# Performance work log

Measured on AMD Instinct MI355X. Metric: run time of the kernel, lower is better.

Reference implementation:

```python
import jax, jax.numpy as jnp
import numpy as np

N_ATOMS = 4096
HSIZE = 128
N_HEADS = 8
D_K = HSIZE // N_HEADS


def setup_inputs() -> dict:
    key = jax.random.key(0)
    ks = jax.random.split(key, 11)
    s = 1.0 / np.sqrt(HSIZE)
    return {
        "query": jax.random.normal(ks[0], (N_ATOMS, HSIZE), dtype=jnp.float32),
        "key": jax.random.normal(ks[1], (N_ATOMS, HSIZE), dtype=jnp.float32),
        "value": jax.random.normal(ks[2], (N_ATOMS, HSIZE), dtype=jnp.float32),
        "mask": jax.random.randint(ks[3], (N_ATOMS, N_ATOMS), 0, 2, dtype=jnp.int32),
        "Wq": jax.random.normal(ks[4], (HSIZE, HSIZE), dtype=jnp.float32) * s,
        "bq": jnp.zeros((HSIZE,), dtype=jnp.float32),
        "Wk": jax.random.normal(ks[5], (HSIZE, HSIZE), dtype=jnp.float32) * s,
        "bk": jnp.zeros((HSIZE,), dtype=jnp.float32),
        "Wv": jax.random.normal(ks[6], (HSIZE, HSIZE), dtype=jnp.float32) * s,
        "bv": jnp.zeros((HSIZE,), dtype=jnp.float32),
        "Wo": jax.random.normal(ks[7], (HSIZE, HSIZE), dtype=jnp.float32) * s,
    }


def _mha(query, key, value, mask, Wq, bq, Wk, bk, Wv, bv, Wo):
    n = query.shape[0]
    # project and split heads: [n, hsize] -> [H, n, d_k]
    def heads(x, W, b):
        return (x @ W.T + b).reshape(n, N_HEADS, D_K).transpose(1, 0, 2)
    q = heads(query, Wq, bq)
    k = heads(key, Wk, bk)
    v = heads(value, Wv, bv)
    scale = 1.0 / jnp.sqrt(jnp.asarray(D_K, q.dtype))
    scores = jnp.einsum("hnd,hmd->hnm", q, k) * scale  # [H, n, n]
    scores = jnp.where(mask[None, :, :] == 0, jnp.asarray(-1e9, scores.dtype), scores)
    p_attn = jax.nn.softmax(scores, axis=-1)
    x = jnp.einsum("hnm,hmd->hnd", p_attn, v)  # [H, n, d_k]
    x = x.transpose(1, 0, 2).reshape(n, HSIZE)  # merge heads
    return x @ Wo.T  # output_linear has bias=False


def reference(query, key, value, mask, Wq, bq, Wk, bk, Wv, bv, Wo):
    return _mha(query, key, value, mask, Wq, bq, Wk, bk, Wv, bv, Wo)
```

## Files before the change

### kernel.cpp

```cpp
#include <hip/hip_runtime.h>

#define NA 4096
#define HS 128
#define PSTR 72
#define CSTR 136

typedef unsigned short u16;
typedef unsigned long long u64;
using bf16x8  = __attribute__((ext_vector_type(8))) short;
using f32x4   = __attribute__((ext_vector_type(4))) float;
using ushort8 = __attribute__((ext_vector_type(8))) unsigned short;

#define QSCALE 0.18033688011112042f

static __device__ __forceinline__ u16 f2bf(float f) {
    unsigned u = __builtin_bit_cast(unsigned, f);
    u += 0x7FFFu + ((u >> 16) & 1u);
    return (u16)(u >> 16);
}

__global__ __launch_bounds__(256) void cvt_w(
    const float* __restrict__ Wq, const float* __restrict__ Wk,
    const float* __restrict__ Wv, const float* __restrict__ Wo,
    const float* __restrict__ bq, const float* __restrict__ bk,
    const float* __restrict__ bv,
    u16* __restrict__ Wf, float* __restrict__ bb)
{
    const int gid = blockIdx.x * 256 + threadIdx.x;
    const int e = gid * 4;
    const int mat = e >> 14, off = e & 16383;
    const float* src = (mat == 0) ? Wq : (mat == 1) ? Wk : (mat == 2) ? Wv : Wo;
    const float s = (mat == 0) ? QSCALE : 1.0f;
    float4 v = *(const float4*)(src + off);
    ushort4 o;
    o.x = f2bf(v.x * s); o.y = f2bf(v.y * s);
    o.z = f2bf(v.z * s); o.w = f2bf(v.w * s);
    const int j = off >> 7, k0 = off & 127;
    const int j0 = j >> 4, c = j & 15, kk = k0 >> 5, q = (k0 >> 3) & 3;
    const int tgt = mat * 16384 + ((j0 * 4 + kk) * 16 + c) * 32 + q * 8 + (k0 & 7);
    *(ushort4*)(Wf + tgt) = o;
    if (gid < 128)      bb[gid] = bq[gid] * QSCALE;
    else if (gid < 256) bb[gid] = bk[gid - 128];
    else if (gid < 384) bb[gid] = bv[gid - 256];
}

__global__ __launch_bounds__(256) void proj_mfma(
    const float* __restrict__ Xq, const float* __restrict__ Xk, const float* __restrict__ Xv,
    const u16* __restrict__ Wf, const float* __restrict__ bb,
    u16* __restrict__ Qbh, u16* __restrict__ Kbh, u16* __restrict__ VtB)
{
    const int mat = blockIdx.y;
    const float* X = (mat == 0) ? Xq : (mat == 1) ? Xk : Xv;
    const u16* Wm = Wf + mat * 16384;
    const float* bm = bb + mat * 128;
    const int r0b = blockIdx.x * 32;

    __shared__ __align__(16) u16 Xs[32 * CSTR];
    __shared__ __align__(16) u16 Cs[32 * CSTR];

    const int t = threadIdx.x;

    {
        const int r = t >> 3, cb = (t & 7) * 16;
        const float* Xr = X + (size_t)(r0b + r) * HS + cb;
#pragma unroll
        for (int seg = 0; seg < 4; ++seg) {
            float4 f = *(const float4*)(Xr + seg * 4);
            ushort4 u;
            u.x = f2bf(f.x); u.y = f2bf(f.y); u.z = f2bf(f.z); u.w = f2bf(f.w);
            *(ushort4*)(Xs + r * CSTR + cb + seg * 4) = u;
        }
    }
    __syncthreads();

    const int wv = t >> 6, lane = t & 63;
    const int c = lane & 15, q = lane >> 4;
    const int rw = (wv & 1) * 16;
    const int j0b = (wv >> 1) * 4;

    bf16x8 af[4];
#pragma unroll
    for (int kk = 0; kk < 4; ++kk)
        af[kk] = *(const bf16x8*)(Xs + (rw + c) * CSTR + kk * 32 + q * 8);

    const f32x4 zero = {0.f, 0.f, 0.f, 0.f};
#pragma unroll
    for (int jj = 0; jj < 4; ++jj) {
        const int j0 = j0b + jj;
        f32x4 acc = zero;
#pragma unroll
        for (int kk = 0; kk < 4; ++kk) {
            bf16x8 bf = *(const bf16x8*)(Wm + (j0 * 4 + kk) * 512 + c * 32 + q * 8);
            acc = __builtin_amdgcn_mfma_f32_16x16x32_bf16(af[kk], bf, acc, 0, 0, 0);
        }
        const float bias = bm[j0 * 16 + c];
#pragma unroll
        for (int r = 0; r < 4; ++r)
            Cs[(rw + 4 * q + r) * CSTR + j0 * 16 + c] = f2bf(acc[r] + bias);
    }
    __syncthreads();

    if (mat < 2) {
        u16* dst = (mat == 0) ? Qbh : Kbh;
        const int h8 = t >> 5, r = t & 31;
        const u16* src = Cs + r * CSTR + h8 * 16;
        u16* dp = dst + (size_t)h8 * (NA * 16) + (size_t)(r0b + r) * 16;
        *(bf16x8*)(dp)     = *(const bf16x8*)(src);
        *(bf16x8*)(dp + 8) = *(const bf16x8*)(src + 8);
    } else {
        const int d = t >> 1, s = t & 1;
        const int kb = r0b >> 6, ko = (r0b & 32) + s * 16;
        ushort8 v0, v1;
#pragma unroll
        for (int jj = 0; jj < 8; ++jj) v0[jj] = Cs[(s * 16 + jj) * CSTR + d];
#pragma unroll
        for (int jj = 0; jj < 8; ++jj) v1[jj] = Cs[(s * 16 + 8 + jj) * CSTR + d];
        u16* dp = VtB + (size_t)kb * 8192 + d * 64 + ko;
        *(ushort8*)(dp)     = v0;
        *(ushort8*)(dp + 8) = v1;
    }
}

__global__ __launch_bounds__(512, 8) void attn(
    const int* __restrict__ mask,
    const u16* __restrict__ Qbh, const u16* __restrict__ Kbh, const u16* __restrict__ VtB,
    float* __restrict__ part)
{
    __shared__ __align__(16) u16 Pbuf[8 * 16 * PSTR];
    __shared__ __align__(8)  u64 Mwp[16 * 17];

    const int t = threadIdx.x;
    const int h = t >> 6;
    const int lane = t & 63;
    const int c = lane & 15;
    const int q = lane >> 4;
    const int tile = blockIdx.x, split = blockIdx.y;
    const int i0 = tile * 16;
    const int kt0 = split * 1024;

#pragma unroll 4
    for (int rr = 0; rr < 32; ++rr) {
        const int idx = h * 32 + rr;
        const int row = idx >> 4, wc = idx & 15;
        const int v = mask[(size_t)(i0 + row) * NA + kt0 + wc * 64 + lane];
        u64 b = __ballot(v != 0);
        if (lane == 0) Mwp[row * 17 + wc] = b;
    }

    const u16* Qh = Qbh + (size_t)h * (NA * 16);
    const u16* Kh = Kbh + (size_t)h * (NA * 16);

    const bf16x8 qf = *(const bf16x8*)(Qh + (size_t)(i0 + c) * 16 + (q & 1) * 8);

    __syncthreads();

    const f32x4 zero = {0.f, 0.f, 0.f, 0.f};
    f32x4 Oacc = zero;
    float lsum = 0.f;
    u16* Pw = Pbuf + h * 16 * PSTR;

#pragma unroll 1
    for (int it = 0; it < 16; ++it) {
        const int kt = kt0 + it * 64;
        const u16* Vb = VtB + (size_t)(kt >> 6) * 8192 + (h * 16 + c) * 64;

        f32x4 ST[4];
#pragma unroll
        for (int t4 = 0; t4 < 4; ++t4) {
            bf16x8 kf = *(const bf16x8*)(Kh + (size_t)(kt + t4 * 16 + c) * 16 + (q & 1) * 8);
            ST[t4] = __builtin_amdgcn_mfma_f32_16x16x32_bf16(kf, qf, zero, 0, 0, 0);
        }
        bf16x8 vf0 = *(const bf16x8*)(Vb + q * 8);
        bf16x8 vf1 = *(const bf16x8*)(Vb + 32 + q * 8);

        u64 w = Mwp[c * 17 + it] >> (4 * q);
        unsigned mlo = (unsigned)w, mhi = (unsigned)(w >> 32);

#pragma unroll
        for (int t4 = 0; t4 < 4; ++t4) {
            const unsigned mw = (t4 < 2) ? mlo : mhi;
            const int sh = (t4 & 1) * 16;
            float p0 = ((mw >> (sh + 0)) & 1) ? __builtin_amdgcn_exp2f(ST[t4][0]) : 0.f;
            float p1 = ((mw >> (sh + 1)) & 1) ? __builtin_amdgcn_exp2f(ST[t4][1]) : 0.f;
            float p2 = ((mw >> (sh + 2)) & 1) ? __builtin_amdgcn_exp2f(ST[t4][2]) : 0.f;
            float p3 = ((mw >> (sh + 3)) & 1) ? __builtin_amdgcn_exp2f(ST[t4][3]) : 0.f;
            lsum += (p0 + p1) + (p2 + p3);
            unsigned lo = ((__builtin_bit_cast(unsigned, p0) + 0x8000u) >> 16)
                        | ((__builtin_bit_cast(unsigned, p1) + 0x8000u) & 0xFFFF0000u);
            unsigned hi = ((__builtin_bit_cast(unsigned, p2) + 0x8000u) >> 16)
                        | ((__builtin_bit_cast(unsigned, p3) + 0x8000u) & 0xFFFF0000u);
            *(uint2*)(Pw + c * PSTR + t4 * 16 + 4 * q) = make_uint2(lo, hi);
        }
        __asm__ volatile("" ::: "memory");
        __builtin_amdgcn_s_waitcnt(0xC07F);
        __asm__ volatile("" ::: "memory");

        bf16x8 pf0 = *(const bf16x8*)(Pw + c * PSTR + q * 8);
        bf16x8 pf1 = *(const bf16x8*)(Pw + c * PSTR + 32 + q * 8);
        Oacc = __builtin_amdgcn_mfma_f32_16x16x32_bf16(pf0, vf0, Oacc, 0, 0, 0);
        Oacc = __builtin_amdgcn_mfma_f32_16x16x32_bf16(pf1, vf1, Oacc, 0, 0, 0);
    }

    lsum += __shfl_xor(lsum, 16, 64);
    lsum += __shfl_xor(lsum, 32, 64);

    float* base = part + (size_t)((tile * 4 + split) * 8 + h) * 272;
#pragma unroll
    for (int r = 0; r < 4; ++r)
        base[(4 * q + r) * 16 + c] = Oacc[r];
    if (q == 0) base[256 + c] = lsum;
}

__global__ __launch_bounds__(256) void reduce_out(
    const float* __restrict__ part, const u16* __restrict__ Wf,
    float* __restrict__ out)
{
    __shared__ __align__(16) u16 xs[16 * CSTR];

    const int t = threadIdx.x;
    const int tile = blockIdx.x;
    const int i0 = tile * 16;
    const float* Pt = part + (size_t)tile * 4 * 8 * 272;

    {
        const int i = t >> 4, d = t & 15;
#pragma unroll
        for (int h = 0; h < 8; ++h) {
            float os = 0.f, ls = 0.f;
#pragma unroll
            for (int s = 0; s < 4; ++s) {
                const float* b = Pt + (size_t)(s * 8 + h) * 272;
                os += b[i * 16 + d];
                ls += b[256 + i];
            }
            xs[i * CSTR + h * 16 + d] = f2bf(os / ls);
        }
    }
    __syncthreads();

    const int wv = t >> 6, lane = t & 63;
    const int c = lane & 15, q = lane >> 4;
    const u16* WoB = Wf + 3 * 16384;

    bf16x8 af[4];
#pragma unroll
    for (int kk = 0; kk < 4; ++kk)
        af[kk] = *(const bf16x8*)(xs + c * CSTR + kk * 32 + q * 8);

    const f32x4 zero = {0.f, 0.f, 0.f, 0.f};
#pragma unroll
    for (int jj = 0; jj < 2; ++jj) {
        const int j0 = wv * 2 + jj;
        f32x4 acc = zero;
#pragma unroll
        for (int kk = 0; kk < 4; ++kk) {
            bf16x8 bf = *(const bf16x8*)(WoB + (j0 * 4 + kk) * 512 + c * 32 + q * 8);
            acc = __builtin_amdgcn_mfma_f32_16x16x32_bf16(af[kk], bf, acc, 0, 0, 0);
        }
#pragma unroll
        for (int r = 0; r < 4; ++r)
            out[(size_t)(i0 + 4 * q + r) * HS + j0 * 16 + c] = acc[r];
    }
}

extern "C" void kernel_launch(void* const* d_in, const int* in_sizes, int n_in,
                              void* d_out, int out_size, void* d_ws, size_t ws_size,
                              hipStream_t stream) {
    const float* query = (const float*)d_in[0];
    const float* key   = (const float*)d_in[1];
    const float* value = (const float*)d_in[2];
    const int*   mask  = (const int*)d_in[3];
    const float* Wq    = (const float*)d_in[4];
    const float* bq    = (const float*)d_in[5];
    const float* Wk    = (const float*)d_in[6];
    const float* bk    = (const float*)d_in[7];
    const float* Wv    = (const float*)d_in[8];
    const float* bv    = (const float*)d_in[9];
    const float* Wo    = (const float*)d_in[10];

    u16* Qbh = (u16*)d_ws;
    u16* Kbh = Qbh + (size_t)NA * HS;
    u16* VtB = Kbh + (size_t)NA * HS;
    u16* Wf  = VtB + (size_t)NA * HS;
    float* bb    = (float*)(Wf + 4 * 16384);
    float* partb = bb + 384;

    cvt_w<<<64, 256, 0, stream>>>(Wq, Wk, Wv, Wo, bq, bk, bv, Wf, bb);
    proj_mfma<<<dim3(128, 3), 256, 0, stream>>>(query, key, value, Wf, bb, Qbh, Kbh, VtB);
    attn<<<dim3(256, 4), 512, 0, stream>>>(mask, Qbh, Kbh, VtB, partb);
    reduce_out<<<256, 256, 0, stream>>>(partb, Wf, (float*)d_out);
}
```

Before: 184.2 us.

## Pre-pack mask bits in a separate pass, prefetch K, move row sums to MFMA

Mask bit-packing moves out of the attention kernel into extra blocks of the weight-conversion kernel, which write a 64-bit-per-64-column bitmap to workspace; attn then loads the small bitmap instead of reading int32 mask rows. K fragments are software-prefetched one iteration ahead. Masking now applies a lookup-table AND after a packed bf16 conversion instead of branchy per-element selects. Row sums come from extra MFMAs against a ones vector rather than scalar adds and shuffles. The mask is still read once in full, now in a separate pass, and the row sums are taken from bf16-rounded probabilities.

```diff
diff --git a/kernel.cpp b/kernel.cpp
--- a/kernel.cpp
+++ b/kernel.cpp
@@ -23,25 +23,40 @@
     const float* __restrict__ Wq, const float* __restrict__ Wk,
     const float* __restrict__ Wv, const float* __restrict__ Wo,
     const float* __restrict__ bq, const float* __restrict__ bk,
-    const float* __restrict__ bv,
-    u16* __restrict__ Wf, float* __restrict__ bb)
+    const float* __restrict__ bv, const int* __restrict__ mask,
+    u16* __restrict__ Wf, float* __restrict__ bb, u64* __restrict__ Mp)
 {
-    const int gid = blockIdx.x * 256 + threadIdx.x;
-    const int e = gid * 4;
-    const int mat = e >> 14, off = e & 16383;
-    const float* src = (mat == 0) ? Wq : (mat == 1) ? Wk : (mat == 2) ? Wv : Wo;
-    const float s = (mat == 0) ? QSCALE : 1.0f;
-    float4 v = *(const float4*)(src + off);
-    ushort4 o;
-    o.x = f2bf(v.x * s); o.y = f2bf(v.y * s);
-    o.z = f2bf(v.z * s); o.w = f2bf(v.w * s);
-    const int j = off >> 7, k0 = off & 127;
-    const int j0 = j >> 4, c = j & 15, kk = k0 >> 5, q = (k0 >> 3) & 3;
-    const int tgt = mat * 16384 + ((j0 * 4 + kk) * 16 + c) * 32 + q * 8 + (k0 & 7);
-    *(ushort4*)(Wf + tgt) = o;
-    if (gid < 128)      bb[gid] = bq[gid] * QSCALE;
-    else if (gid < 256) bb[gid] = bk[gid - 128];
-    else if (gid < 384) bb[gid] = bv[gid - 256];
+    const int bx = blockIdx.x;
+    const int t = threadIdx.x;
+    if (bx < 64) {
+        const int gid = bx * 256 + t;
+        const int e = gid * 4;
+        const int mat = e >> 14, off = e & 16383;
+        const float* src = (mat == 0) ? Wq : (mat == 1) ? Wk : (mat == 2) ? Wv : Wo;
+        const float s = (mat == 0) ? QSCALE : 1.0f;
+        float4 v = *(const float4*)(src + off);
+        ushort4 o;
+        o.x = f2bf(v.x * s); o.y = f2bf(v.y * s);
+        o.z = f2bf(v.z * s); o.w = f2bf(v.w * s);
+        const int j = off >> 7, k0 = off & 127;
+        const int j0 = j >> 4, c = j & 15, kk = k0 >> 5, q = (k0 >> 3) & 3;
+        const int tgt = mat * 16384 + ((j0 * 4 + kk) * 16 + c) * 32 + q * 8 + (k0 & 7);
+        *(ushort4*)(Wf + tgt) = o;
+        if (gid < 128)      bb[gid] = bq[gid] * QSCALE;
+        else if (gid < 256) bb[gid] = bk[gid - 128];
+        else if (gid < 384) bb[gid] = bv[gid - 256];
+    } else {
+        const int mb = bx - 64;
+        const int wv = t >> 6, lane = t & 63;
+        const int row = mb * 4 + wv;
+        const int* mrow = mask + (size_t)row * NA;
+        u64* orow = Mp + (size_t)row * 64;
+#pragma unroll 8
+        for (int w = 0; w < 64; ++w) {
+            u64 b = __ballot(mrow[w * 64 + lane] != 0);
+            if (lane == 0) orow[w] = b;
+        }
+    }
 }
 
 __global__ __launch_bounds__(256) void proj_mfma(
@@ -122,12 +137,13 @@
 }
 
 __global__ __launch_bounds__(512, 8) void attn(
-    const int* __restrict__ mask,
+    const u64* __restrict__ Mp,
     const u16* __restrict__ Qbh, const u16* __restrict__ Kbh, const u16* __restrict__ VtB,
     float* __restrict__ part)
 {
     __shared__ __align__(16) u16 Pbuf[8 * 16 * PSTR];
     __shared__ __align__(8)  u64 Mwp[16 * 17];
+    __shared__ __align__(8)  u64 Mtab[16];
 
     const int t = threadIdx.x;
     const int h = t >> 6;
@@ -138,13 +154,14 @@
     const int i0 = tile * 16;
     const int kt0 = split * 1024;
 
-#pragma unroll 4
-    for (int rr = 0; rr < 32; ++rr) {
-        const int idx = h * 32 + rr;
-        const int row = idx >> 4, wc = idx & 15;
-        const int v = mask[(size_t)(i0 + row) * NA + kt0 + wc * 64 + lane];
-        u64 b = __ballot(v != 0);
-        if (lane == 0) Mwp[row * 17 + wc] = b;
+    if (t < 256) {
+        const int row = t >> 4, w = t & 15;
+        Mwp[row * 17 + w] = Mp[(size_t)(i0 + row) * 64 + (kt0 >> 6) + w];
+    }
+    if (t < 16) {
+        const unsigned lo = ((t & 1) ? 0xFFFFu : 0u) | ((t & 2) ? 0xFFFF0000u : 0u);
+        const unsigned hi = ((t & 4) ? 0xFFFFu : 0u) | ((t & 8) ? 0xFFFF0000u : 0u);
+        Mtab[t] = (u64)lo | ((u64)hi << 32);
     }
 
     const u16* Qh = Qbh + (size_t)h * (NA * 16);
@@ -152,26 +169,39 @@
 
     const bf16x8 qf = *(const bf16x8*)(Qh + (size_t)(i0 + c) * 16 + (q & 1) * 8);
 
+    bf16x8 ones;
+#pragma unroll
+    for (int i = 0; i < 8; ++i) ones[i] = (short)0x3F80;
+
     __syncthreads();
 
     const f32x4 zero = {0.f, 0.f, 0.f, 0.f};
     f32x4 Oacc = zero;
-    float lsum = 0.f;
+    f32x4 Lacc = zero;
     u16* Pw = Pbuf + h * 16 * PSTR;
+
+    bf16x8 kf[4];
+#pragma unroll
+    for (int t4 = 0; t4 < 4; ++t4)
+        kf[t4] = *(const bf16x8*)(Kh + (size_t)(kt0 + t4 * 16 + c) * 16 + (q & 1) * 8);
 
 #pragma unroll 1
     for (int it = 0; it < 16; ++it) {
         const int kt = kt0 + it * 64;
         const u16* Vb = VtB + (size_t)(kt >> 6) * 8192 + (h * 16 + c) * 64;
 
-        f32x4 ST[4];
-#pragma unroll
-        for (int t4 = 0; t4 < 4; ++t4) {
-            bf16x8 kf = *(const bf16x8*)(Kh + (size_t)(kt + t4 * 16 + c) * 16 + (q & 1) * 8);
-            ST[t4] = __builtin_amdgcn_mfma_f32_16x16x32_bf16(kf, qf, zero, 0, 0, 0);
-        }
         bf16x8 vf0 = *(const bf16x8*)(Vb + q * 8);
         bf16x8 vf1 = *(const bf16x8*)(Vb + 32 + q * 8);
+
+        f32x4 ST[4];
+#pragma unroll
+        for (int t4 = 0; t4 < 4; ++t4)
+            ST[t4] = __builtin_amdgcn_mfma_f32_16x16x32_bf16(kf[t4], qf, zero, 0, 0, 0);
+
+        const int ktn = kt0 + ((it + 1) & 15) * 64;
+#pragma unroll
+        for (int t4 = 0; t4 < 4; ++t4)
+            kf[t4] = *(const bf16x8*)(Kh + (size_t)(ktn + t4 * 16 + c) * 16 + (q & 1) * 8);
 
         u64 w = Mwp[c * 17 + it] >> (4 * q);
         unsigned mlo = (unsigned)w, mhi = (unsigned)(w >> 32);
@@ -180,15 +210,17 @@
         for (int t4 = 0; t4 < 4; ++t4) {
             const unsigned mw = (t4 < 2) ? mlo : mhi;
             const int sh = (t4 & 1) * 16;
-            float p0 = ((mw >> (sh + 0)) & 1) ? __builtin_amdgcn_exp2f(ST[t4][0]) : 0.f;
-            float p1 = ((mw >> (sh + 1)) & 1) ? __builtin_amdgcn_exp2f(ST[t4][1]) : 0.f;
-            float p2 = ((mw >> (sh + 2)) & 1) ? __builtin_amdgcn_exp2f(ST[t4][2]) : 0.f;
-            float p3 = ((mw >> (sh + 3)) & 1) ? __builtin_amdgcn_exp2f(ST[t4][3]) : 0.f;
-            lsum += (p0 + p1) + (p2 + p3);
-            unsigned lo = ((__builtin_bit_cast(unsigned, p0) + 0x8000u) >> 16)
-                        | ((__builtin_bit_cast(unsigned, p1) + 0x8000u) & 0xFFFF0000u);
-            unsigned hi = ((__builtin_bit_cast(unsigned, p2) + 0x8000u) >> 16)
-                        | ((__builtin_bit_cast(unsigned, p3) + 0x8000u) & 0xFFFF0000u);
+            const unsigned nib = (mw >> sh) & 15u;
+            float p0 = __builtin_amdgcn_exp2f(ST[t4][0]);
+            float p1 = __builtin_amdgcn_exp2f(ST[t4][1]);
+            float p2 = __builtin_amdgcn_exp2f(ST[t4][2]);
+            float p3 = __builtin_amdgcn_exp2f(ST[t4][3]);
+            unsigned lo, hi;
+            asm("v_cvt_pk_bf16_f32 %0, %1, %2" : "=v"(lo) : "v"(p0), "v"(p1));
+            asm("v_cvt_pk_bf16_f32 %0, %1, %2" : "=v"(hi) : "v"(p2), "v"(p3));
+            const u64 mex = Mtab[nib];
+            lo &= (unsigned)mex;
+            hi &= (unsigned)(mex >> 32);
             *(uint2*)(Pw + c * PSTR + t4 * 16 + 4 * q) = make_uint2(lo, hi);
         }
         __asm__ volatile("" ::: "memory");
@@ -199,16 +231,19 @@
         bf16x8 pf1 = *(const bf16x8*)(Pw + c * PSTR + 32 + q * 8);
         Oacc = __builtin_amdgcn_mfma_f32_16x16x32_bf16(pf0, vf0, Oacc, 0, 0, 0);
         Oacc = __builtin_amdgcn_mfma_f32_16x16x32_bf16(pf1, vf1, Oacc, 0, 0, 0);
-    }
-
-    lsum += __shfl_xor(lsum, 16, 64);
-    lsum += __shfl_xor(lsum, 32, 64);
+        Lacc = __builtin_amdgcn_mfma_f32_16x16x32_bf16(pf0, ones, Lacc, 0, 0, 0);
+        Lacc = __builtin_amdgcn_mfma_f32_16x16x32_bf16(pf1, ones, Lacc, 0, 0, 0);
+    }
 
     float* base = part + (size_t)((tile * 4 + split) * 8 + h) * 272;
 #pragma unroll
     for (int r = 0; r < 4; ++r)
         base[(4 * q + r) * 16 + c] = Oacc[r];
-    if (q == 0) base[256 + c] = lsum;
+    if (c == 0) {
+#pragma unroll
+        for (int r = 0; r < 4; ++r)
+            base[256 + 4 * q + r] = Lacc[r];
+    }
 }
 
 __global__ __launch_bounds__(256) void reduce_out(
@@ -283,10 +318,11 @@
     u16* VtB = Kbh + (size_t)NA * HS;
     u16* Wf  = VtB + (size_t)NA * HS;
     float* bb    = (float*)(Wf + 4 * 16384);
-    float* partb = bb + 384;
-
-    cvt_w<<<64, 256, 0, stream>>>(Wq, Wk, Wv, Wo, bq, bk, bv, Wf, bb);
+    u64*  Mp    = (u64*)(bb + 384);
+    float* partb = (float*)(Mp + (size_t)NA * 64);
+
+    cvt_w<<<64 + 1024, 256, 0, stream>>>(Wq, Wk, Wv, Wo, bq, bk, bv, mask, Wf, bb, Mp);
     proj_mfma<<<dim3(128, 3), 256, 0, stream>>>(query, key, value, Wf, bb, Qbh, Kbh, VtB);
-    attn<<<dim3(256, 4), 512, 0, stream>>>(mask, Qbh, Kbh, VtB, partb);
+    attn<<<dim3(256, 4), 512, 0, stream>>>(Mp, Qbh, Kbh, VtB, partb);
     reduce_out<<<256, 256, 0, stream>>>(partb, Wf, (float*)d_out);
 }
```

Result: slower. 203.0 us (+10.2%).
